# Kernel optimization log

Hardware: AMD Instinct MI355X
Metric: run time of the kernel (lower is better)

Reference implementation:

```python
import jax, jax.numpy as jnp
import numpy as np

EPS = 1e-08

def setup_inputs() -> dict:
    key = jax.random.key(0)
    k1, k2, k3 = jax.random.split(key, 3)
    b, cin, cout, ksz, h, w = 16, 256, 256, 3, 64, 64
    return {
        "x": jax.random.normal(k1, (b, cin, h, w), dtype=jnp.float32),
        "s": jax.random.normal(k2, (b, cin), dtype=jnp.float32),
        "weight": jax.random.normal(k3, (cout, cin, ksz, ksz), dtype=jnp.float32),
    }

def reference(x, s, weight):
    # x: [b, cin, h, w]; s: [b, cin]; weight: [cout, cin, k, k]
    b, cin, h, w = x.shape
    cout, _, ksz, _ = weight.shape
    pad = ksz // 2
    # demodulate pre-normalization of weight and style
    wn = weight * jax.lax.rsqrt(jnp.mean(jnp.square(weight), axis=(1, 2, 3), keepdims=True))
    sn = s * jax.lax.rsqrt(jnp.mean(jnp.square(s)))
    # per-sample modulation: [b, cout, cin, k, k]
    wmod = wn[None, :, :, :, :] * sn[:, None, :, None, None]
    # demodulation: normalize each output filter per sample
    sigma_inv = jax.lax.rsqrt(jnp.sum(jnp.square(wmod), axis=(2, 3, 4), keepdims=True) + EPS)
    wmod = wmod * sigma_inv
    # batch-grouped conv: input [1, b*cin, h, w], weight [b*cout, cin, k, k]
    xg = x.reshape(1, b * cin, h, w)
    wg = wmod.reshape(b * cout, cin, ksz, ksz)
    y = jax.lax.conv_general_dilated(
        xg, wg,
        window_strides=(1, 1),
        padding=[(pad, pad), (pad, pad)],
        feature_group_count=b,
        dimension_numbers=("NCHW", "OIHW", "NCHW"),
    )
    return y.reshape(b, cout, h, w)
```

## Files before the change

### kernel.cpp

```cpp
#include <hip/hip_runtime.h>
#include <hip/hip_bf16.h>

#define EPS 1e-8f
#define B_  16
#define CIN 256
#define COUT 256
#define HW 64

typedef __bf16 bf16x8 __attribute__((ext_vector_type(8)));
typedef float  f32x4  __attribute__((ext_vector_type(4)));

__device__ __forceinline__ void async16(void* lds, const void* g) {
    __builtin_amdgcn_global_load_lds(
        (const __attribute__((address_space(1))) unsigned int*)g,
        (__attribute__((address_space(3))) unsigned int*)lds,
        16, 0, 0);
}

__device__ __forceinline__ uint pack2(float lo, float hi) {
    __bf16 a = (__bf16)lo, b = (__bf16)hi;
    unsigned short ua = __builtin_bit_cast(unsigned short, a);
    unsigned short ub = __builtin_bit_cast(unsigned short, b);
    return ((uint)ub << 16) | (uint)ua;
}

__global__ __launch_bounds__(256) void prep_kernel(const float* __restrict__ x,
                                                   const float* __restrict__ s,
                                                   const float* __restrict__ w,
                                                   __bf16* __restrict__ xbf,
                                                   __bf16* __restrict__ wfull,
                                                   __bf16* __restrict__ zrow) {
    __shared__ uint xsd[64 * 159];
    __shared__ float red[8];
    const int bid = blockIdx.x;
    const int t   = threadIdx.x;

    if (bid == 1024) {
        uint4 z = make_uint4(0, 0, 0, 0);
        uint4* zp = (uint4*)zrow;
#pragma unroll
        for (int k = 0; k < 9; ++k) zp[k * 256 + t] = z;
        return;
    }

    if (bid > 1024) {
        const int co = bid - 1025;
        const int ci = t;
        const int lane = t & 63, wid = t >> 6;
        float as = 0.f;
#pragma unroll
        for (int k = 0; k < 16; ++k) { float sv = s[k * 256 + t]; as += sv * sv; }
        const float* wp = w + ((size_t)co * CIN + ci) * 9;
        float wv[9];
        float q = 0.f;
#pragma unroll
        for (int tp = 0; tp < 9; ++tp) { wv[tp] = wp[tp]; q += wv[tp] * wv[tp]; }
        float a = as, qq = q;
        for (int off = 32; off > 0; off >>= 1) {
            a  += __shfl_down(a,  off, 64);
            qq += __shfl_down(qq, off, 64);
        }
        if (lane == 0) { red[wid] = a; red[4 + wid] = qq; }
        __syncthreads();
        const float ssum = red[0] + red[1] + red[2] + red[3];
        const float Sw   = red[4] + red[5] + red[6] + red[7];
        const float sn2  = (float)(B_ * CIN) / ssum;
        const float wn   = rsqrtf(Sw / 2304.f);
        const float wn2sn2 = wn * wn * sn2;
        const float wsn  = wn * sqrtf(sn2);

        for (int b = 0; b < B_; ++b) {
            const float sv = s[b * CIN + ci];
            float v = sv * sv * q;
            for (int off = 32; off > 0; off >>= 1) v += __shfl_down(v, off, 64);
            __syncthreads();
            if (lane == 0) red[wid] = v;
            __syncthreads();
            const float S = red[0] + red[1] + red[2] + red[3];
            const float coef = wsn * rsqrtf(wn2sn2 * S + EPS);
            const float sc = sv * coef;
            const size_t obase = ((size_t)b * 9) * 65536 + (size_t)(ci >> 5) * 8192
                               + (size_t)co * 32 + (ci & 31);
#pragma unroll
            for (int tap = 0; tap < 9; ++tap)
                wfull[obase + (size_t)tap * 65536] = (__bf16)(wv[tap] * sc);
        }
        return;
    }

    const int row = bid & 63;
    const int b   = bid >> 6;
    const float* xbase = x + ((size_t)b * CIN * HW + row) * HW;
#pragma unroll
    for (int k = 0; k < 8; ++k) {
        int p   = k * 256 + t;
        int ci2 = p >> 4;
        int c4  = (p & 15) * 4;
        const float* src = xbase + (size_t)(2 * ci2) * (HW * HW) + c4;
        float4 v0 = *(const float4*)src;
        float4 v1 = *(const float4*)(src + HW * HW);
        const int dj = ci2 + (ci2 >> 2);
#pragma unroll
        for (int i = 0; i < 4; ++i)
            xsd[(c4 + i) * 159 + dj] = pack2((&v0.x)[i], (&v1.x)[i]);
    }
    __syncthreads();
    __bf16* orow = xbf + (((size_t)b * HW + row) * 64) * CIN;
#pragma unroll
    for (int k = 0; k < 8; ++k) {
        int o   = k * 256 + t;
        int col = o >> 5;
        int u   = o & 31;
        const uint* rp = &xsd[col * 159 + 5 * u];
        uint4 vv; vv.x = rp[0]; vv.y = rp[1]; vv.z = rp[2]; vv.w = rp[3];
        *(uint4*)&orow[(size_t)col * CIN + u * 8] = vv;
    }
}

__global__ __launch_bounds__(256, 2) void conv_mfma4(const __bf16* __restrict__ xbf,
                                                     const __bf16* __restrict__ zrow,
                                                     const __bf16* __restrict__ wfull,
                                                     float* __restrict__ out) {
    __shared__ __attribute__((aligned(16))) __bf16 xs[2][1056 * 8];

    const int bid = blockIdx.x;
    const int b   = (bid & 7) + ((bid >= 256) ? 8 : 0);
    const int r0  = ((bid >> 3) & 31) * 2;
    const int t = threadIdx.x;
    const int wy = t >> 6, lane = t & 63;
    const int m16 = lane & 15, q = lane >> 4;

    const __bf16* gsrc[5];
#pragma unroll
    for (int i = 0; i < 5; ++i) {
        int qq, rem;
        if (i < 4) { qq = i;  rem = t; }
        else       { qq = wy; rem = 256 + (lane & 7); }
        int irow = rem / 66;
        int col  = rem - irow * 66;
        int gr   = r0 - 1 + irow;
        if ((unsigned)gr < 64u && col != 0 && col != 65)
            gsrc[i] = xbf + (((size_t)b * HW + gr) * 64 + (col - 1)) * CIN + qq * 8;
        else
            gsrc[i] = zrow + col * CIN + qq * 8;
    }

#pragma unroll
    for (int i = 0; i < 4; ++i)
        async16((char*)xs[0] + (i * 264 + t) * 16, gsrc[i]);
    if (lane < 8)
        async16((char*)xs[0] + (wy * 264 + 256 + lane) * 16, gsrc[4]);

    f32x4 acc[4][8] = {};
    const __bf16* abase = wfull + (size_t)b * 589824
                        + (size_t)(wy * 64 + m16) * 32 + q * 8;

    bf16x8 afc[4];
#pragma unroll
    for (int i = 0; i < 4; ++i)
        afc[i] = *(const bf16x8*)(abase + i * 512);

    for (int cc = 0; cc < 8; ++cc) {
        const __bf16* wb = abase + (size_t)cc * 8192;
        __syncthreads();
        if (cc < 7) {
            const int d = cc * 32 + 32;
#pragma unroll
            for (int i = 0; i < 4; ++i)
                async16((char*)xs[(cc + 1) & 1] + (i * 264 + t) * 16, gsrc[i] + d);
            if (lane < 8)
                async16((char*)xs[(cc + 1) & 1] + (wy * 264 + 256 + lane) * 16, gsrc[4] + d);
        }
        const __bf16* xcur = xs[cc & 1];
#pragma unroll
        for (int tap = 0; tap < 9; ++tap) {
            const int dr = tap / 3, dc = tap % 3;
            bf16x8 bfr[8];
#pragma unroll
            for (int j = 0; j < 8; ++j) {
                const int slot = q * 264 + ((j >> 2) + dr) * 66 + (j & 3) * 16 + m16 + dc;
                bfr[j] = *(const bf16x8*)&xcur[slot * 8];
            }
            bf16x8 afn[4];
            if (tap < 8) {
#pragma unroll
                for (int i = 0; i < 4; ++i)
                    afn[i] = *(const bf16x8*)(wb + (size_t)(tap + 1) * 65536 + i * 512);
            } else if (cc < 7) {
#pragma unroll
                for (int i = 0; i < 4; ++i)
                    afn[i] = *(const bf16x8*)(wb + 8192 + i * 512);
            }
            __builtin_amdgcn_s_setprio(1);
#pragma unroll
            for (int i = 0; i < 4; ++i)
#pragma unroll
                for (int j = 0; j < 8; ++j)
                    acc[i][j] = __builtin_amdgcn_mfma_f32_16x16x32_bf16(afc[i], bfr[j], acc[i][j], 0, 0, 0);
            __builtin_amdgcn_s_setprio(0);
            if (tap < 8 || cc < 7) {
#pragma unroll
                for (int i = 0; i < 4; ++i) afc[i] = afn[i];
            }
        }
    }

#pragma unroll
    for (int i = 0; i < 4; ++i) {
        const int cobase = wy * 64 + i * 16 + q * 4;
#pragma unroll
        for (int reg = 0; reg < 4; ++reg) {
            float* op = out + ((size_t)b * COUT + (cobase + reg)) * (HW * HW) + r0 * HW + m16;
#pragma unroll
            for (int j = 0; j < 8; ++j)
                op[(j >> 2) * HW + (j & 3) * 16] = acc[i][j][reg];
        }
    }
}

extern "C" void kernel_launch(void* const* d_in, const int* in_sizes, int n_in,
                              void* d_out, int out_size, void* d_ws, size_t ws_size,
                              hipStream_t stream) {
    const float* x = (const float*)d_in[0];
    const float* s = (const float*)d_in[1];
    const float* w = (const float*)d_in[2];
    float* out = (float*)d_out;

    float* ws = (float*)d_ws;
    __bf16* wfull = (__bf16*)(ws + 70656);
    __bf16* zrow  = (__bf16*)(ws + 4789248);
    __bf16* xbf   = (__bf16*)(ws + 4798464);

    prep_kernel<<<1281, 256, 0, stream>>>(x, s, w, xbf, wfull, zrow);
    conv_mfma4<<<512, 256, 0, stream>>>(xbf, zrow, wfull, out);
}
```

Before: 183.1 us.

## Split conv output channels across blocks and halve per-wave accumulator tile

The conv kernel now splits the 256 output channels into two halves across blocks, doubling the grid to 1024. Each wave computes a 64-channel by one-row tile instead of 64 channels by two rows. This halves the accumulator registers so the launch bound can be raised to four blocks per CU for more occupancy. It also removes the software prefetch of the next tap's weight fragments. In exchange each input tile is loaded into LDS twice across blocks, there are fewer MFMAs per loaded fragment, and weight-load latency is no longer hidden explicitly.

```diff
diff --git a/kernel.cpp b/kernel.cpp
--- a/kernel.cpp
+++ b/kernel.cpp
@@ -117,18 +117,22 @@
     }
 }
 
-__global__ __launch_bounds__(256, 2) void conv_mfma4(const __bf16* __restrict__ xbf,
+__global__ __launch_bounds__(256, 4) void conv_mfma7(const __bf16* __restrict__ xbf,
                                                      const __bf16* __restrict__ zrow,
                                                      const __bf16* __restrict__ wfull,
                                                      float* __restrict__ out) {
     __shared__ __attribute__((aligned(16))) __bf16 xs[2][1056 * 8];
 
     const int bid = blockIdx.x;
-    const int b   = (bid & 7) + ((bid >= 256) ? 8 : 0);
-    const int r0  = ((bid >> 3) & 31) * 2;
+    const int b   = (bid & 7) + ((bid >= 512) ? 8 : 0);
+    const int idx = (bid >> 3) & 63;
+    const int r0  = (idx & 31) * 2;
+    const int coh = idx >> 5;
     const int t = threadIdx.x;
     const int wy = t >> 6, lane = t & 63;
     const int m16 = lane & 15, q = lane >> 4;
+    const int wr  = wy >> 1;
+    const int co0 = coh * 128 + (wy & 1) * 64;
 
     const __bf16* gsrc[5];
 #pragma unroll
@@ -151,14 +155,9 @@
     if (lane < 8)
         async16((char*)xs[0] + (wy * 264 + 256 + lane) * 16, gsrc[4]);
 
-    f32x4 acc[4][8] = {};
+    f32x4 acc[4][4] = {};
     const __bf16* abase = wfull + (size_t)b * 589824
-                        + (size_t)(wy * 64 + m16) * 32 + q * 8;
-
-    bf16x8 afc[4];
-#pragma unroll
-    for (int i = 0; i < 4; ++i)
-        afc[i] = *(const bf16x8*)(abase + i * 512);
+                        + (size_t)(co0 + m16) * 32 + q * 8;
 
     for (int cc = 0; cc < 8; ++cc) {
         const __bf16* wb = abase + (size_t)cc * 8192;
@@ -175,45 +174,35 @@
 #pragma unroll
         for (int tap = 0; tap < 9; ++tap) {
             const int dr = tap / 3, dc = tap % 3;
-            bf16x8 bfr[8];
-#pragma unroll
-            for (int j = 0; j < 8; ++j) {
-                const int slot = q * 264 + ((j >> 2) + dr) * 66 + (j & 3) * 16 + m16 + dc;
+            bf16x8 afc[4], bfr[4];
+#pragma unroll
+            for (int i = 0; i < 4; ++i)
+                afc[i] = *(const bf16x8*)(wb + (size_t)tap * 65536 + i * 512);
+#pragma unroll
+            for (int j = 0; j < 4; ++j) {
+                const int slot = q * 264 + (wr + dr) * 66 + j * 16 + m16 + dc;
                 bfr[j] = *(const bf16x8*)&xcur[slot * 8];
             }
-            bf16x8 afn[4];
-            if (tap < 8) {
+            __builtin_amdgcn_s_setprio(1);
+#pragma unroll
+            for (int j = 0; j < 4; ++j)
 #pragma unroll
                 for (int i = 0; i < 4; ++i)
-                    afn[i] = *(const bf16x8*)(wb + (size_t)(tap + 1) * 65536 + i * 512);
-            } else if (cc < 7) {
-#pragma unroll
-                for (int i = 0; i < 4; ++i)
-                    afn[i] = *(const bf16x8*)(wb + 8192 + i * 512);
-            }
-            __builtin_amdgcn_s_setprio(1);
-#pragma unroll
-            for (int i = 0; i < 4; ++i)
-#pragma unroll
-                for (int j = 0; j < 8; ++j)
                     acc[i][j] = __builtin_amdgcn_mfma_f32_16x16x32_bf16(afc[i], bfr[j], acc[i][j], 0, 0, 0);
             __builtin_amdgcn_s_setprio(0);
-            if (tap < 8 || cc < 7) {
-#pragma unroll
-                for (int i = 0; i < 4; ++i) afc[i] = afn[i];
-            }
         }
     }
 
 #pragma unroll
     for (int i = 0; i < 4; ++i) {
-        const int cobase = wy * 64 + i * 16 + q * 4;
+        const int cobase = co0 + i * 16 + q * 4;
 #pragma unroll
         for (int reg = 0; reg < 4; ++reg) {
-            float* op = out + ((size_t)b * COUT + (cobase + reg)) * (HW * HW) + r0 * HW + m16;
-#pragma unroll
-            for (int j = 0; j < 8; ++j)
-                op[(j >> 2) * HW + (j & 3) * 16] = acc[i][j][reg];
+            float* op = out + ((size_t)b * COUT + (cobase + reg)) * (HW * HW)
+                      + (r0 + wr) * HW + m16;
+#pragma unroll
+            for (int j = 0; j < 4; ++j)
+                op[j * 16] = acc[i][j][reg];
         }
     }
 }
@@ -232,5 +221,5 @@
     __bf16* xbf   = (__bf16*)(ws + 4798464);
 
     prep_kernel<<<1281, 256, 0, stream>>>(x, s, w, xbf, wfull, zrow);
-    conv_mfma4<<<512, 256, 0, stream>>>(xbf, zrow, wfull, out);
-}
+    conv_mfma7<<<1024, 256, 0, stream>>>(xbf, zrow, wfull, out);
+}
```

New measurement: 211.4 us. 15.4% more time.
